# Optimization experiments

Hardware: AMD Instinct MI355X
Metric: run time of the kernel (lower is better)

## Reference

```python
import jax, jax.numpy as jnp
import numpy as np

NUM_EMBEDDINGS = 4096
EMBEDDING_DIM = 64
COMMITMENT_LOSS_FACTOR = 0.25


def setup_inputs() -> dict:
    key = jax.random.key(0)
    k1, k2 = jax.random.split(key)
    z = jax.random.normal(k1, (16, 64, 64, EMBEDDING_DIM), dtype=jnp.float32)
    init_range = 1.0 / NUM_EMBEDDINGS
    embeddings = jax.random.uniform(
        k2, (NUM_EMBEDDINGS, EMBEDDING_DIM), dtype=jnp.float32,
        minval=-init_range, maxval=init_range)
    return {"z": z, "embeddings": embeddings}


def reference(z, embeddings):
    # z: [B, H, W, D] channels-last latents; embeddings: [K, D] codebook
    B, H, W, D = z.shape
    z_flat = z.reshape(-1, D)  # [N, D]
    # Squared Euclidean distances (argmin-equivalent to cdist p=2, sqrt is monotone)
    d2 = (jnp.sum(z_flat * z_flat, axis=1, keepdims=True)
          - 2.0 * (z_flat @ embeddings.T)
          + jnp.sum(embeddings * embeddings, axis=1))  # [N, K]
    closest = jnp.argmin(d2, axis=1)  # [N]
    quantized = embeddings[closest].reshape(z.shape)  # gather == one_hot @ embeddings
    quantized_indices = closest.reshape(B, H, W)
    # eval-mode forward (no EMA buffer update)
    commitment_loss = jnp.sum((jax.lax.stop_gradient(quantized) - z) ** 2)
    loss = COMMITMENT_LOSS_FACTOR * commitment_loss
    quantized = z + jax.lax.stop_gradient(quantized - z)  # straight-through
    return (quantized.transpose(0, 3, 1, 2),      # [B, D, H, W]
            quantized_indices[:, None, :, :],      # [B, 1, H, W]
            loss)
```

## Files before the change

### kernel.cpp

```cpp
#include <hip/hip_runtime.h>


typedef _Float16 half8 __attribute__((ext_vector_type(8)));
typedef float f32x4 __attribute__((ext_vector_type(4)));

#define NCODES 4096
#define DIM 64
#define NROWS 65536
#define OUT_IDX_OFF 4194304
#define OUT_LOSS_OFF 4259840

#define WS_EHI   0u
#define WS_EE    524288u
#define WS_RLOSS 540672u
#define WS_TU1   802816u
#define WS_TK1   1327104u
#define WS_TU2   1851392u
#define WS_TK23  2375680u
#define WS_TU3   2899968u
#define WS_TU4   3424256u
#define WS_LISTB 3948544u
#define WS_CNTB  4210688u
#define WS_PART  4210944u

__device__ __forceinline__ float pairwise_sumsq64(const float* v) {
    float r[8];
#pragma unroll
    for (int j = 0; j < 8; ++j) r[j] = __fmul_rn(v[j], v[j]);
#pragma unroll
    for (int m = 1; m < 8; ++m) {
#pragma unroll
        for (int j = 0; j < 8; ++j)
            r[j] = __fadd_rn(r[j], __fmul_rn(v[8 * m + j], v[8 * m + j]));
    }
    float s01 = __fadd_rn(r[0], r[1]);
    float s23 = __fadd_rn(r[2], r[3]);
    float s45 = __fadd_rn(r[4], r[5]);
    float s67 = __fadd_rn(r[6], r[7]);
    return __fadd_rn(__fadd_rn(s01, s23), __fadd_rn(s45, s67));
}

__device__ __forceinline__ float exact_d2(const float* __restrict__ emb, int k,
                                          const float* zr, float zz, float eev) {
    const float4* ep = reinterpret_cast<const float4*>(emb + (size_t)k * DIM);
    float da = 0.f;
#pragma unroll
    for (int q = 0; q < 16; ++q) {
        float4 A = ep[q];
        da += A.x * zr[4 * q + 0]; da += A.y * zr[4 * q + 1];
        da += A.z * zr[4 * q + 2]; da += A.w * zr[4 * q + 3];
    }
    return __fadd_rn(__fsub_rn(zz, __fmul_rn(2.0f, da)), eev);
}

__device__ __forceinline__ void gload_lds16(const void* g, void* l) {
    __builtin_amdgcn_global_load_lds(
        (const __attribute__((address_space(1))) unsigned int*)g,
        (__attribute__((address_space(3))) unsigned int*)l, 16, 0, 0);
}

#define WAITVM(n)                                               \
    {                                                           \
        asm volatile("s_waitcnt vmcnt(" #n ")" ::: "memory");   \
        __builtin_amdgcn_sched_barrier(0);                      \
    }

__global__ void vq_prep(const float* __restrict__ emb, _Float16* __restrict__ ehi,
                        float* __restrict__ ee) {
    int k = blockIdx.x * 256 + threadIdx.x;
    float v[DIM];
    const float4* p = reinterpret_cast<const float4*>(emb + (size_t)k * DIM);
#pragma unroll
    for (int i = 0; i < 16; ++i) {
        float4 a = p[i];
        v[4 * i + 0] = a.x; v[4 * i + 1] = a.y; v[4 * i + 2] = a.z; v[4 * i + 3] = a.w;
    }
    ee[k] = pairwise_sumsq64(v);
#pragma unroll
    for (int i = 0; i < 8; ++i) {
        half8 h;
#pragma unroll
        for (int j = 0; j < 8; ++j) h[j] = (_Float16)(v[8 * i + j] * 256.0f);
        *reinterpret_cast<half8*>(ehi + (size_t)k * DIM + 8 * i) = h;
    }
}

#define INS4MAX(x, xid, s)                                    \
    {                                                         \
        bool q1 = (x) > M1[s], q2 = (x) > M2[s], q3 = (x) > M3[s]; \
        M4[s] = q3 ? M3[s] : fmaxf((x), M4[s]);               \
        M3[s] = q2 ? M2[s] : (q3 ? (x) : M3[s]);              \
        G3[s] = q2 ? G2[s] : (q3 ? (xid) : G3[s]);            \
        M2[s] = q1 ? M1[s] : (q2 ? (x) : M2[s]);              \
        G2[s] = q1 ? G1[s] : (q2 ? (xid) : G2[s]);            \
        M1[s] = q1 ? (x) : M1[s];                             \
        G1[s] = q1 ? (xid) : G1[s];                           \
    }

__launch_bounds__(256, 4)
__global__ void vq_scan(const float* __restrict__ z, const _Float16* __restrict__ ehi,
                        float* __restrict__ tU1, int* __restrict__ tK1,
                        float* __restrict__ tU2, int* __restrict__ tK23,
                        float* __restrict__ tU3, float* __restrict__ tU4) {
    __shared__ float4 sB[4][512];

    const int tid = threadIdx.x;
    const int lane = tid & 63;
    const int w = tid >> 6;
    const int rlo = lane & 15;
    const int quad = lane >> 4;
    const int half = blockIdx.y;
    const int rowbase = blockIdx.x * 128 + w * 32;

    half8 zhi[2][2];
#pragma unroll
    for (int rt = 0; rt < 2; ++rt) {
        const float* zp = z + (size_t)(rowbase + rt * 16 + rlo) * DIM + quad * 8;
#pragma unroll
        for (int ks = 0; ks < 2; ++ks) {
            float4 a = *reinterpret_cast<const float4*>(zp + ks * 32);
            float4 b = *reinterpret_cast<const float4*>(zp + ks * 32 + 4);
            float f[8] = {a.x, a.y, a.z, a.w, b.x, b.y, b.z, b.w};
            half8 hi;
#pragma unroll
            for (int e = 0; e < 8; ++e) hi[e] = (_Float16)f[e];
            zhi[rt][ks] = hi;
        }
    }

    int gOff[2];
#pragma unroll
    for (int i = 0; i < 2; ++i) {
        int L = tid + i * 256;
        int T = L >> 6, u = L & 63;
        int code = (T >> 1) * 16 + (u & 15);
        int dg = (T & 1) * 4 + (u >> 4);
        gOff[i] = (code * 8 + dg) * 16;
    }
    const char* srcHiB = (const char*)ehi + (size_t)half * 2048 * 128;

    auto issue = [&](int cc, int bb) {
        const char* hs = srcHiB + (size_t)cc * 8192;
        char* dH = (char*)&sB[bb][0];
#pragma unroll
        for (int i = 0; i < 2; ++i)
            gload_lds16(hs + gOff[i], dH + (tid + i * 256) * 16);
    };

    issue(0, 0);
    issue(1, 1);

    float M1[2], M2[2], M3[2], M4[2];
    int G1[2], G2[2], G3[2];
#pragma unroll
    for (int s = 0; s < 2; ++s) {
        M1[s] = -3e38f; M2[s] = -3e38f; M3[s] = -3e38f; M4[s] = -3e38f;
        G1[s] = 0; G2[s] = 0; G3[s] = 0;
    }
    const f32x4 zero4 = {0.f, 0.f, 0.f, 0.f};

#pragma unroll 1
    for (int c = 0; c < 32; ++c) {
        if (c < 30) {
            issue(c + 2, (c + 2) & 3);
            WAITVM(4);
        } else if (c == 30) {
            WAITVM(2);
        } else {
            WAITVM(0);
        }
        __builtin_amdgcn_s_barrier();
        __builtin_amdgcn_sched_barrier(0);

        const float4* bh = sB[c & 3];
        float run[2];
#pragma unroll
        for (int s = 0; s < 2; ++s) run[s] = -3e38f;
#pragma unroll
        for (int t = 0; t < 4; ++t) {
            half8 a0h = __builtin_bit_cast(half8, bh[(t * 2 + 0) * 64 + lane]);
            half8 a1h = __builtin_bit_cast(half8, bh[(t * 2 + 1) * 64 + lane]);
#pragma unroll
            for (int rt = 0; rt < 2; ++rt) {
                f32x4 acc = __builtin_amdgcn_mfma_f32_16x16x32_f16(a0h, zhi[rt][0], zero4, 0, 0, 0);
                acc = __builtin_amdgcn_mfma_f32_16x16x32_f16(a1h, zhi[rt][1], acc, 0, 0, 0);
                run[rt] = fmaxf(run[rt],
                                fmaxf(fmaxf(acc[0], acc[1]), fmaxf(acc[2], acc[3])));
            }
        }
        const int gb = (c << 6) + (quad << 2);
#pragma unroll
        for (int s = 0; s < 2; ++s) INS4MAX(run[s], gb, s);
        __builtin_amdgcn_sched_barrier(0);
    }

#pragma unroll
    for (int s = 0; s < 2; ++s) {
#pragma unroll
        for (int d = 16; d < 64; d <<= 1) {
            float o1 = __shfl_xor(M1[s], d); int p1 = __shfl_xor(G1[s], d);
            float o2 = __shfl_xor(M2[s], d); int p2 = __shfl_xor(G2[s], d);
            float o3 = __shfl_xor(M3[s], d); int p3 = __shfl_xor(G3[s], d);
            float o4 = __shfl_xor(M4[s], d);
            INS4MAX(o1, p1, s);
            INS4MAX(o2, p2, s);
            INS4MAX(o3, p3, s);
            M4[s] = fmaxf(M4[s], o4);
        }
    }

    if (lane < 16) {
        const int hoff = half << 11;
#pragma unroll
        for (int s = 0; s < 2; ++s) {
            int grow = rowbase + s * 16 + lane;
            size_t idx = (size_t)half * NROWS + grow;
            tU1[idx] = M1[s] * -0.0078125f;
            tU2[idx] = M2[s] * -0.0078125f;
            tU3[idx] = M3[s] * -0.0078125f;
            tU4[idx] = M4[s] * -0.0078125f;
            tK1[idx] = G1[s] + hoff;
            tK23[idx] = (G2[s] + hoff) | ((G3[s] + hoff) << 16);
        }
    }
}

__global__ void vq_finish(const float* __restrict__ z, const float* __restrict__ emb,
                          const float* __restrict__ ee,
                          const float* __restrict__ tU1, const int* __restrict__ tK1,
                          const float* __restrict__ tU2, const int* __restrict__ tK23,
                          const float* __restrict__ tU3, const float* __restrict__ tU4,
                          float* __restrict__ out, float* __restrict__ rowloss,
                          int* __restrict__ listB, int* __restrict__ cntB,
                          double* __restrict__ part) {
    __shared__ double sd[256];
    const int tid = threadIdx.x;
    const int row = blockIdx.x * 256 + tid;

    float u1 = tU1[row]; int g1 = tK1[row];
    float u2 = tU2[row];
    float u3 = tU3[row]; float u4 = tU4[row];
    int k23 = tK23[row];
    int g2 = k23 & 0xFFFF, g3 = ((unsigned)k23) >> 16;
    {
        float b1 = tU1[NROWS + row]; int h1 = tK1[NROWS + row];
        float b2 = tU2[NROWS + row];
        float b3 = tU3[NROWS + row]; float b4 = tU4[NROWS + row];
        int hk = tK23[NROWS + row];
        int h2 = hk & 0xFFFF, h3 = ((unsigned)hk) >> 16;
#define INSU(bv, bi)                                           \
        { bool q1 = (bv) < u1, q2 = (bv) < u2, q3 = (bv) < u3; \
          u4 = q3 ? u3 : fminf((bv), u4);                      \
          u3 = q2 ? u2 : (q3 ? (bv) : u3);                     \
          g3 = q2 ? g2 : (q3 ? (bi) : g3);                     \
          u2 = q1 ? u1 : (q2 ? (bv) : u2);                     \
          g2 = q1 ? g1 : (q2 ? (bi) : g2);                     \
          u1 = q1 ? (bv) : u1;                                 \
          g1 = q1 ? (bi) : g1; }
        INSU(b1, h1);
        INSU(b2, h2);
        INSU(b3, h3);
        u4 = fminf(u4, b4);
#undef INSU
    }

    float zr[DIM];
    {
        const float4* zp = reinterpret_cast<const float4*>(z + (size_t)row * DIM);
#pragma unroll
        for (int i = 0; i < 16; ++i) {
            float4 a = zp[i];
            zr[4 * i + 0] = a.x; zr[4 * i + 1] = a.y; zr[4 * i + 2] = a.z; zr[4 * i + 3] = a.w;
        }
    }
    float zzs = 0.f;
#pragma unroll
    for (int i = 0; i < DIM; ++i) zzs = fmaf(zr[i], zr[i], zzs);

    float delta = ((zzs > 120.f) ? 3.4e-5f : 1.7e-5f) + 2.5e-5f;

    if (u4 - u1 < delta) {
        int p = atomicAdd(cntB, 1);
        listB[p] = row;
    }

    const float zz = pairwise_sumsq64(zr);
    float best = 3e38f; int kb = 0x7fffffff;
    int secs[3]; int nsec = 1; secs[0] = g1;
    if (u2 - u1 < delta) {
        secs[1] = g2; nsec = 2;
        if (u3 - u1 < delta) { secs[2] = g3; nsec = 3; }
    }
    for (int si = 0; si < nsec; ++si) {
        const int base = secs[si];
#pragma unroll
        for (int t = 0; t < 4; ++t) {
#pragma unroll
            for (int j = 0; j < 4; ++j) {
                int k = base + t * 16 + j;
                float d2 = exact_d2(emb, k, zr, zz, ee[k]);
                if (d2 < best || (d2 == best && k < kb)) { best = d2; kb = k; }
            }
        }
    }

    const int bimg = row >> 12, hw = row & 4095;
    float* o = out + (size_t)bimg * 262144 + hw;
    const float4* qp = reinterpret_cast<const float4*>(emb + (size_t)kb * DIM);
    float loss = 0.f;
#pragma unroll
    for (int i = 0; i < 16; ++i) {
        float4 q = qp[i];
        float qs[4] = {q.x, q.y, q.z, q.w};
#pragma unroll
        for (int j = 0; j < 4; ++j) {
            float dif = qs[j] - zr[4 * i + j];
            loss = fmaf(dif, dif, loss);
            o[(size_t)(4 * i + j) * 4096] = qs[j];
        }
    }
    rowloss[row] = loss;
    out[OUT_IDX_OFF + row] = (float)kb;

    sd[tid] = (double)loss;
    __syncthreads();
    for (int st = 128; st > 0; st >>= 1) {
        if (tid < st) sd[tid] += sd[tid + st];
        __syncthreads();
    }
    if (tid == 0) part[blockIdx.x] = sd[0];
}

__global__ void vq_fallback(const float* __restrict__ z, const float* __restrict__ emb,
                            const float* __restrict__ ee, const int* __restrict__ listB,
                            const int* __restrict__ cntB, float* __restrict__ out,
                            const float* __restrict__ rowloss, double* __restrict__ part) {
    __shared__ float sZ[DIM];
    __shared__ unsigned long long sK[4];
    __shared__ int sKb;
    const int n = *cntB;
    const int tid = threadIdx.x;
    const int lane = tid & 63;
    const int w = tid >> 6;

    for (int i = blockIdx.x; i < n; i += 1024) {
        const int row = listB[i];
        __syncthreads();
        if (tid < DIM) sZ[tid] = z[(size_t)row * DIM + tid];
        __syncthreads();
        float zr[DIM];
#pragma unroll
        for (int q = 0; q < DIM; ++q) zr[q] = sZ[q];
        const float zz = pairwise_sumsq64(zr);

        unsigned long long best = ~0ull;
#pragma unroll 1
        for (int j = 0; j < 16; ++j) {
            int c = tid + j * 256;
            float d2 = exact_d2(emb, c, zr, zz, ee[c]);
            unsigned long long key =
                (((unsigned long long)__float_as_uint(d2)) << 32) | (unsigned)c;
            best = key < best ? key : best;
        }
#pragma unroll
        for (int d = 1; d < 64; d <<= 1) {
            unsigned long long o2 = __shfl_xor(best, d);
            best = o2 < best ? o2 : best;
        }
        if (lane == 0) sK[w] = best;
        __syncthreads();
        if (tid == 0) {
            unsigned long long b = sK[0];
            b = sK[1] < b ? sK[1] : b;
            b = sK[2] < b ? sK[2] : b;
            b = sK[3] < b ? sK[3] : b;
            sKb = (int)(b & 0xFFFFFFFFu);
        }
        __syncthreads();
        const int kb = sKb;
        if (tid < DIM) {
            const float qv = emb[(size_t)kb * DIM + tid];
            const float zv = sZ[tid];
            int bimg = row >> 12, hw = row & 4095;
            out[(size_t)bimg * 262144 + (size_t)tid * 4096 + hw] = qv;
            float lp = (qv - zv) * (qv - zv);
#pragma unroll
            for (int d = 1; d < 64; d <<= 1) lp += __shfl_xor(lp, d);
            if (tid == 0) {
                double dl = (double)lp - (double)rowloss[row];
                atomicAdd(&part[row >> 8], dl);
                out[OUT_IDX_OFF + row] = (float)kb;
            }
        }
    }
}

__global__ void vq_red2(const double* __restrict__ part, float* __restrict__ out_loss) {
    __shared__ double sd[256];
    sd[threadIdx.x] = part[threadIdx.x];
    __syncthreads();
    for (int st = 128; st > 0; st >>= 1) {
        if (threadIdx.x < st) sd[threadIdx.x] += sd[threadIdx.x + st];
        __syncthreads();
    }
    if (threadIdx.x == 0) out_loss[0] = (float)(0.25 * sd[0]);
}

extern "C" void kernel_launch(void* const* d_in, const int* in_sizes, int n_in,
                              void* d_out, int out_size, void* d_ws, size_t ws_size,
                              hipStream_t stream) {
    const float* z = (const float*)d_in[0];
    const float* emb = (const float*)d_in[1];
    float* out = (float*)d_out;
    char* ws = (char*)d_ws;

    _Float16* ehi = (_Float16*)(ws + WS_EHI);
    float* ee = (float*)(ws + WS_EE);
    float* rowloss = (float*)(ws + WS_RLOSS);
    float* tU1 = (float*)(ws + WS_TU1);
    int*   tK1 = (int*)(ws + WS_TK1);
    float* tU2 = (float*)(ws + WS_TU2);
    int*   tK23 = (int*)(ws + WS_TK23);
    float* tU3 = (float*)(ws + WS_TU3);
    float* tU4 = (float*)(ws + WS_TU4);
    int* listB = (int*)(ws + WS_LISTB);
    int* cntB  = (int*)(ws + WS_CNTB);
    double* part = (double*)(ws + WS_PART);

    hipMemsetAsync(cntB, 0, sizeof(int), stream);
    vq_prep<<<NCODES / 256, 256, 0, stream>>>(emb, ehi, ee);
    vq_scan<<<dim3(NROWS / 128, 2), 256, 0, stream>>>(z, ehi, tU1, tK1, tU2, tK23, tU3, tU4);
    vq_finish<<<NROWS / 256, 256, 0, stream>>>(z, emb, ee, tU1, tK1, tU2, tK23, tU3, tU4,
                                               out, rowloss, listB, cntB, part);
    vq_fallback<<<1024, 256, 0, stream>>>(z, emb, ee, listB, cntB, out, rowloss, part);
    vq_red2<<<1, 256, 0, stream>>>(part, out + OUT_LOSS_OFF);
}
```

Measured before the change: 168.2 us.

## Split each finish row across four threads with shared-memory z staging

The finish kernel now assigns four threads per row instead of one. The z row is loaded cooperatively and coalesced into shared memory, then each thread scores a quarter of the candidate codes. A packed 64-bit (distance, index) key is reduced with shuffles and each thread writes a quarter of the output channels. This aims to cut per-thread serial work and uncoalesced z loads in the tail kernel. The price is four times as many blocks, redundant per-thread register copies of z, an extra memset and double atomics into the partial sums. The packed-key min keeps the lowest-index tie-break only because the distances are non-negative floats.

```diff
diff --git a/kernel.cpp b/kernel.cpp
--- a/kernel.cpp
+++ b/kernel.cpp
@@ -225,6 +225,7 @@
     }
 }
 
+__launch_bounds__(256, 4)
 __global__ void vq_finish(const float* __restrict__ z, const float* __restrict__ emb,
                           const float* __restrict__ ee,
                           const float* __restrict__ tU1, const int* __restrict__ tK1,
@@ -233,9 +234,19 @@
                           float* __restrict__ out, float* __restrict__ rowloss,
                           int* __restrict__ listB, int* __restrict__ cntB,
                           double* __restrict__ part) {
+    __shared__ float zs[64][68];
     __shared__ double sd[256];
     const int tid = threadIdx.x;
-    const int row = blockIdx.x * 256 + tid;
+    const int rl = tid >> 2;
+    const int j = tid & 3;
+    const int row = blockIdx.x * 64 + rl;
+
+    {
+        const float4* zp = reinterpret_cast<const float4*>(z + (size_t)row * DIM + j * 16);
+        float4 c0 = zp[0], c1 = zp[1], c2 = zp[2], c3 = zp[3];
+        float4* dst = reinterpret_cast<float4*>(&zs[rl][j * 16]);
+        dst[0] = c0; dst[1] = c1; dst[2] = c2; dst[3] = c3;
+    }
 
     float u1 = tU1[row]; int g1 = tK1[row];
     float u2 = tU2[row];
@@ -264,9 +275,11 @@
 #undef INSU
     }
 
+    __syncthreads();
+
     float zr[DIM];
     {
-        const float4* zp = reinterpret_cast<const float4*>(z + (size_t)row * DIM);
+        const float4* zp = reinterpret_cast<const float4*>(&zs[rl][0]);
 #pragma unroll
         for (int i = 0; i < 16; ++i) {
             float4 a = zp[i];
@@ -279,13 +292,13 @@
 
     float delta = ((zzs > 120.f) ? 3.4e-5f : 1.7e-5f) + 2.5e-5f;
 
-    if (u4 - u1 < delta) {
+    if (j == 0 && u4 - u1 < delta) {
         int p = atomicAdd(cntB, 1);
         listB[p] = row;
     }
 
     const float zz = pairwise_sumsq64(zr);
-    float best = 3e38f; int kb = 0x7fffffff;
+    unsigned long long bestkey = ~0ull;
     int secs[3]; int nsec = 1; secs[0] = g1;
     if (u2 - u1 < delta) {
         secs[1] = g2; nsec = 2;
@@ -295,40 +308,51 @@
         const int base = secs[si];
 #pragma unroll
         for (int t = 0; t < 4; ++t) {
-#pragma unroll
-            for (int j = 0; j < 4; ++j) {
-                int k = base + t * 16 + j;
-                float d2 = exact_d2(emb, k, zr, zz, ee[k]);
-                if (d2 < best || (d2 == best && k < kb)) { best = d2; kb = k; }
-            }
-        }
-    }
+            int k = base + t * 16 + j;
+            float d2 = exact_d2(emb, k, zr, zz, ee[k]);
+            unsigned long long key =
+                (((unsigned long long)__float_as_uint(d2)) << 32) | (unsigned)k;
+            bestkey = key < bestkey ? key : bestkey;
+        }
+    }
+    {
+        unsigned long long o1 = __shfl_xor(bestkey, 1);
+        bestkey = o1 < bestkey ? o1 : bestkey;
+        unsigned long long o2 = __shfl_xor(bestkey, 2);
+        bestkey = o2 < bestkey ? o2 : bestkey;
+    }
+    const int kb = (int)(bestkey & 0xFFFFFFFFu);
 
     const int bimg = row >> 12, hw = row & 4095;
     float* o = out + (size_t)bimg * 262144 + hw;
-    const float4* qp = reinterpret_cast<const float4*>(emb + (size_t)kb * DIM);
-    float loss = 0.f;
-#pragma unroll
-    for (int i = 0; i < 16; ++i) {
-        float4 q = qp[i];
-        float qs[4] = {q.x, q.y, q.z, q.w};
-#pragma unroll
-        for (int j = 0; j < 4; ++j) {
-            float dif = qs[j] - zr[4 * i + j];
-            loss = fmaf(dif, dif, loss);
-            o[(size_t)(4 * i + j) * 4096] = qs[j];
-        }
-    }
-    rowloss[row] = loss;
-    out[OUT_IDX_OFF + row] = (float)kb;
-
-    sd[tid] = (double)loss;
+    const float4* qp = reinterpret_cast<const float4*>(emb + (size_t)kb * DIM + j * 16);
+    float lp = 0.f;
+#pragma unroll
+    for (int q = 0; q < 4; ++q) {
+        float4 qq = qp[q];
+        float qs[4] = {qq.x, qq.y, qq.z, qq.w};
+#pragma unroll
+        for (int e = 0; e < 4; ++e) {
+            int d = j * 16 + q * 4 + e;
+            float dif = qs[e] - zr[d];
+            lp = fmaf(dif, dif, lp);
+            o[(size_t)d * 4096] = qs[e];
+        }
+    }
+    lp += __shfl_xor(lp, 1);
+    lp += __shfl_xor(lp, 2);
+    if (j == 0) {
+        rowloss[row] = lp;
+        out[OUT_IDX_OFF + row] = (float)kb;
+    }
+
+    sd[tid] = (j == 0) ? (double)lp : 0.0;
     __syncthreads();
     for (int st = 128; st > 0; st >>= 1) {
         if (tid < st) sd[tid] += sd[tid + st];
         __syncthreads();
     }
-    if (tid == 0) part[blockIdx.x] = sd[0];
+    if (tid == 0) atomicAdd(&part[blockIdx.x >> 2], sd[0]);
 }
 
 __global__ void vq_fallback(const float* __restrict__ z, const float* __restrict__ emb,
@@ -428,10 +452,11 @@
     double* part = (double*)(ws + WS_PART);
 
     hipMemsetAsync(cntB, 0, sizeof(int), stream);
+    hipMemsetAsync(part, 0, 256 * sizeof(double), stream);
     vq_prep<<<NCODES / 256, 256, 0, stream>>>(emb, ehi, ee);
     vq_scan<<<dim3(NROWS / 128, 2), 256, 0, stream>>>(z, ehi, tU1, tK1, tU2, tK23, tU3, tU4);
-    vq_finish<<<NROWS / 256, 256, 0, stream>>>(z, emb, ee, tU1, tK1, tU2, tK23, tU3, tU4,
-                                               out, rowloss, listB, cntB, part);
+    vq_finish<<<NROWS / 64, 256, 0, stream>>>(z, emb, ee, tU1, tK1, tU2, tK23, tU3, tU4,
+                                              out, rowloss, listB, cntB, part);
     vq_fallback<<<1024, 256, 0, stream>>>(z, emb, ee, listB, cntB, out, rowloss, part);
     vq_red2<<<1, 256, 0, stream>>>(part, out + OUT_LOSS_OFF);
 }
```

After: 301.2 us. 1.79x slower.

## Split quantized output emission into separate kernel with shared-memory transpose

Applied to the files above, without the earlier changes.

Moves the gather of the chosen codebook rows, the transposed output write and the loss computation out of vq_finish into a new vq_emit kernel. vq_emit stages z and the quantized rows in padded shared memory so that both the reads and the channel-major output stores are coalesced. The old per-thread strided stores were uncoalesced. The change adds an extra kernel launch, a memset and double atomics for the loss partials. It also re-reads the indices from the output buffer, and the fallback kernel must still patch any rows it recomputes.

```diff
diff --git a/kernel.cpp b/kernel.cpp
--- a/kernel.cpp
+++ b/kernel.cpp
@@ -230,12 +230,9 @@
                           const float* __restrict__ tU1, const int* __restrict__ tK1,
                           const float* __restrict__ tU2, const int* __restrict__ tK23,
                           const float* __restrict__ tU3, const float* __restrict__ tU4,
-                          float* __restrict__ out, float* __restrict__ rowloss,
-                          int* __restrict__ listB, int* __restrict__ cntB,
-                          double* __restrict__ part) {
-    __shared__ double sd[256];
-    const int tid = threadIdx.x;
-    const int row = blockIdx.x * 256 + tid;
+                          float* __restrict__ out,
+                          int* __restrict__ listB, int* __restrict__ cntB) {
+    const int row = blockIdx.x * 256 + threadIdx.x;
 
     float u1 = tU1[row]; int g1 = tK1[row];
     float u2 = tU2[row];
@@ -303,32 +300,72 @@
             }
         }
     }
-
-    const int bimg = row >> 12, hw = row & 4095;
-    float* o = out + (size_t)bimg * 262144 + hw;
-    const float4* qp = reinterpret_cast<const float4*>(emb + (size_t)kb * DIM);
-    float loss = 0.f;
-#pragma unroll
-    for (int i = 0; i < 16; ++i) {
-        float4 q = qp[i];
-        float qs[4] = {q.x, q.y, q.z, q.w};
-#pragma unroll
-        for (int j = 0; j < 4; ++j) {
-            float dif = qs[j] - zr[4 * i + j];
-            loss = fmaf(dif, dif, loss);
-            o[(size_t)(4 * i + j) * 4096] = qs[j];
-        }
-    }
-    rowloss[row] = loss;
     out[OUT_IDX_OFF + row] = (float)kb;
-
-    sd[tid] = (double)loss;
+}
+
+__launch_bounds__(256, 4)
+__global__ void vq_emit(const float* __restrict__ z, const float* __restrict__ emb,
+                        float* __restrict__ out, float* __restrict__ rowloss,
+                        double* __restrict__ part) {
+    __shared__ float zs[64 * 65];
+    __shared__ float qs[64 * 65];
+    __shared__ float ls[64 * 5];
+    const int tid = threadIdx.x;
+    const int rl = tid >> 2;
+    const int j = tid & 3;
+    const int row = blockIdx.x * 64 + rl;
+
+    {
+        const float4* zp = reinterpret_cast<const float4*>(
+            z + (size_t)blockIdx.x * 4096 + (size_t)tid * 16);
+        float4 a = zp[0], b = zp[1], c = zp[2], d = zp[3];
+        float v[16] = {a.x, a.y, a.z, a.w, b.x, b.y, b.z, b.w,
+                       c.x, c.y, c.z, c.w, d.x, d.y, d.z, d.w};
+        float* dst = &zs[rl * 65 + j * 16];
+#pragma unroll
+        for (int i = 0; i < 16; ++i) dst[i] = v[i];
+    }
+    {
+        const int kb = (int)out[OUT_IDX_OFF + row];
+        const float4* qp = reinterpret_cast<const float4*>(
+            emb + (size_t)kb * DIM + j * 16);
+        float4 a = qp[0], b = qp[1], c = qp[2], d = qp[3];
+        float v[16] = {a.x, a.y, a.z, a.w, b.x, b.y, b.z, b.w,
+                       c.x, c.y, c.z, c.w, d.x, d.y, d.z, d.w};
+        float* dst = &qs[rl * 65 + j * 16];
+#pragma unroll
+        for (int i = 0; i < 16; ++i) dst[i] = v[i];
+    }
     __syncthreads();
-    for (int st = 128; st > 0; st >>= 1) {
-        if (tid < st) sd[tid] += sd[tid + st];
-        __syncthreads();
-    }
-    if (tid == 0) part[blockIdx.x] = sd[0];
+
+    const int hw_l = tid & 63;
+    const int w = tid >> 6;
+    const int bimg = row >> 12;
+    const int hwb = (blockIdx.x * 64) & 4095;
+    float* ob = out + (size_t)bimg * 262144 + hwb + hw_l;
+    float lp = 0.f;
+#pragma unroll
+    for (int k = 0; k < 16; ++k) {
+        const int d = w * 16 + k;
+        float qv = qs[hw_l * 65 + d];
+        float zv = zs[hw_l * 65 + d];
+        float df = qv - zv;
+        lp = fmaf(df, df, lp);
+        ob[(size_t)d * 4096] = qv;
+    }
+    ls[hw_l * 5 + w] = lp;
+    __syncthreads();
+
+    if (tid < 64) {
+        float r01 = ls[tid * 5 + 0] + ls[tid * 5 + 1];
+        float r23 = ls[tid * 5 + 2] + ls[tid * 5 + 3];
+        float rsum = r01 + r23;
+        rowloss[blockIdx.x * 64 + tid] = rsum;
+        double s = (double)rsum;
+#pragma unroll
+        for (int d = 1; d < 64; d <<= 1) s += __shfl_xor(s, d);
+        if (tid == 0) atomicAdd(&part[blockIdx.x >> 2], s);
+    }
 }
 
 __global__ void vq_fallback(const float* __restrict__ z, const float* __restrict__ emb,
@@ -428,10 +465,12 @@
     double* part = (double*)(ws + WS_PART);
 
     hipMemsetAsync(cntB, 0, sizeof(int), stream);
+    hipMemsetAsync(part, 0, 256 * sizeof(double), stream);
     vq_prep<<<NCODES / 256, 256, 0, stream>>>(emb, ehi, ee);
     vq_scan<<<dim3(NROWS / 128, 2), 256, 0, stream>>>(z, ehi, tU1, tK1, tU2, tK23, tU3, tU4);
     vq_finish<<<NROWS / 256, 256, 0, stream>>>(z, emb, ee, tU1, tK1, tU2, tK23, tU3, tU4,
-                                               out, rowloss, listB, cntB, part);
+                                               out, listB, cntB);
+    vq_emit<<<NROWS / 64, 256, 0, stream>>>(z, emb, out, rowloss, part);
     vq_fallback<<<1024, 256, 0, stream>>>(z, emb, ee, listB, cntB, out, rowloss, part);
     vq_red2<<<1, 256, 0, stream>>>(part, out + OUT_LOSS_OFF);
 }
```

Result: slower. 181.0 us (+7.6%).
